# Optimization experiments

Measured on AMD Instinct MI355X. Metric: run time of the kernel, lower is better.

Reference implementation:

```python
import jax, jax.numpy as jnp
import numpy as np

RES = 0.1
TABLE = 1 << 20  # hash_table_size, power of two
PRIMES = np.array([73856093, 19349669, 83492791], dtype=np.int64)
FEAT_DIM = 120
BMIN = (-2.6, -8.1, 0.0)
BMAX = (4.6, 4.7, 3.1)
M_QUERIES = 1_000_000
CORNERS = np.array([[0,0,0],[1,0,0],[0,1,0],[0,0,1],[1,1,0],[1,0,1],[0,1,1],[1,1,1]], dtype=np.int32)


def _build_table():
    # Replicates build_hash_grid(): first-come voxel index per hash slot, collisions skipped.
    xs = np.arange(BMIN[0], BMAX[0], RES, dtype=np.float32)
    ys = np.arange(BMIN[1], BMAX[1], RES, dtype=np.float32)
    zs = np.arange(BMIN[2], BMAX[2], RES, dtype=np.float32)
    gx, gy, gz = np.meshgrid(xs, ys, zs, indexing='ij')
    coords = np.stack([gx, gy, gz], -1).reshape(-1, 3)
    gc = np.floor(coords / RES).astype(np.int64)
    h = np.remainder((gc * PRIMES).sum(-1), TABLE)
    n = coords.shape[0]
    buf = np.full(TABLE, -1, dtype=np.int32)
    buf[h[::-1]] = np.arange(n, dtype=np.int32)[::-1]
    return buf, n


def setup_inputs() -> dict:
    key = jax.random.key(0)
    k1, k2 = jax.random.split(key)
    buf, n_vox = _build_table()
    lo = jnp.array(BMIN, jnp.float32)
    hi = jnp.array(BMAX, jnp.float32)
    query_pts = lo + (hi - lo) * jax.random.uniform(k1, (M_QUERIES, 3), dtype=jnp.float32)
    features = 0.01 * jax.random.normal(k2, (n_vox, FEAT_DIM), dtype=jnp.float32)
    return {
        "query_pts": query_pts,
        "features": features,
        "buffer_voxel_index": jnp.asarray(buf),  # int32 [TABLE]
    }


def reference(query_pts, features, buffer_voxel_index):
    """query_voxel_feature with trilinear_feat=True: 8-corner hash lookup + trilinear blend."""
    primes_u = jnp.asarray(PRIMES.astype(np.uint32))
    gcf = query_pts / RES                        # [M,3]
    floor = jnp.floor(gcf)
    frac = gcf - floor                           # [M,3]
    base = floor.astype(jnp.int32)               # [M,3]
    acc = jnp.zeros((query_pts.shape[0], features.shape[1]), dtype=features.dtype)
    for c in CORNERS:                            # fixed 8-iteration corner loop
        cj = jnp.asarray(c)
        cc = base + cj                           # [M,3]
        # TABLE is a power of two, so low-20-bits of wrapping uint32 arithmetic
        # equals the exact int64 remainder used by torch.
        h = ((cc.astype(jnp.uint32) * primes_u).sum(-1) & (TABLE - 1)).astype(jnp.int32)
        vidx = buffer_voxel_index[h]             # [M], -1 for empty slots
        w = jnp.where(cj == 0, 1.0 - frac, frac).prod(-1)  # [M] trilinear weight
        w = jnp.where(vidx >= 0, w, 0.0)
        acc = acc + features[jnp.maximum(vidx, 0)] * w[:, None]
    return acc
```

## Files before the change

kernel.cpp:

```cpp
#include <hip/hip_runtime.h>


#define TABLE_MASK ((1u << 20) - 1u)
#define FEAT_DIM 120
#define ROW_STRIDE 120
#define NROWS 75
#define NCHUNK 30
#define NXCD 8
#define C8 32

#define NBINS_X 32
#define NBINS_Y 64
#define NBINS_Z 16
#define NBINS (NBINS_X * NBINS_Y * NBINS_Z)

typedef float f4 __attribute__((ext_vector_type(4)));

__device__ __forceinline__ int query_key_from_pt(float px, float py, float pz) {
    const int bx = (int)floorf(px / 0.1f);
    const int by = (int)floorf(py / 0.1f);
    const int bz = (int)floorf(pz / 0.1f);
    const int kx = ((bx + 32) >> 2) & (NBINS_X - 1);
    const int ky = ((by + 96) >> 2) & (NBINS_Y - 1);
    const int kz = (bz >> 1) & (NBINS_Z - 1);
    return ((kx * NBINS_Y) + ky) * NBINS_Z + kz;
}

__global__ __launch_bounds__(256) void zero_kernel(int* __restrict__ hist8) {
    const int i = blockIdx.x * blockDim.x + threadIdx.x;
    if (i < NXCD * NBINS + 1) hist8[i] = 0;
}

__global__ __launch_bounds__(256) void bin_kernel(
    const float* __restrict__ qp, int* __restrict__ hist8,
    f4* __restrict__ sq8, f4* __restrict__ ovf, int Cr, int M)
{
    const int q = blockIdx.x * blockDim.x + threadIdx.x;
    if (q >= M) return;

    int xcd;
    asm volatile("s_getreg_b32 %0, hwreg(HW_REG_XCC_ID)" : "=s"(xcd));
    xcd &= (NXCD - 1);

    const float px = qp[3 * q + 0];
    const float py = qp[3 * q + 1];
    const float pz = qp[3 * q + 2];
    const int key = query_key_from_pt(px, py, pz);

    const int pos = __hip_atomic_fetch_add(&hist8[xcd * NBINS + key], 1,
                                           __ATOMIC_RELAXED,
                                           __HIP_MEMORY_SCOPE_WORKGROUP);
    f4 s;
    s.x = px; s.y = py; s.z = pz; s.w = __int_as_float(q);
    if (pos < Cr) {
        sq8[((size_t)xcd * NBINS + key) * C8 + pos] = s;
    } else {
        const int o = atomicAdd(&hist8[NXCD * NBINS], 1);
        if (o < M) ovf[o] = s;
    }
}

__global__ __launch_bounds__(512) void voxel_trilinear_kernel(
    const f4*    __restrict__ sq8,
    const float* __restrict__ feat,
    const int*   __restrict__ table,
    const int*   __restrict__ hist8,
    float*       __restrict__ out,
    int Cr)
{
    const int x = blockIdx.x & 7, sblk = blockIdx.x >> 3;
    const int wg = (x + ((sblk >> 7) << 3)) * 128 + (sblk & 127);

    __shared__ int   cnt_s[NXCD];
    __shared__ int   pre_s[NXCD + 1];
    __shared__ int   vox[NROWS];
    __shared__ f4    sqL[NXCD * C8];
    __shared__ float rows[NROWS * ROW_STRIDE];

    const int t = threadIdx.x;

    if (t < NXCD) {
        int c = hist8[t * NBINS + wg];
        cnt_s[t] = (c > Cr) ? Cr : c;
    }
    __syncthreads();
    if (t == 0) {
        int acc = 0;
        pre_s[0] = 0;
#pragma unroll
        for (int i = 0; i < NXCD; ++i) { acc += cnt_s[i]; pre_s[i + 1] = acc; }
    }
    __syncthreads();
    const int total = pre_s[NXCD];
    if (total == 0) return;

    const int binx = wg >> 10;
    const int biny = (wg >> 4) & 63;
    const int binz = wg & 15;
    const int vx0 = binx * 4 - 32;
    const int vy0 = biny * 4 - 96;
    const int vz0 = binz * 2;

    if (t < NROWS) {
        const int i = t / 15;
        const int j = (t / 3) % 5;
        const int k = t % 3;
        const unsigned h = (unsigned)(vx0 + i) * 73856093u
                         + (unsigned)(vy0 + j) * 19349669u
                         + (unsigned)(vz0 + k) * 83492791u;
        vox[t] = table[h & TABLE_MASK];
    }
    {
        const int w = t >> 6;
        const int lane = t & 63;
        if (lane < cnt_s[w])
            sqL[pre_s[w] + lane] = sq8[((size_t)w * NBINS + wg) * C8 + lane];
    }
    __syncthreads();

    for (int idx = t; idx < NROWS * NCHUNK; idx += 512) {
        const int row = idx / NCHUNK;
        const int chunk = idx - row * NCHUNK;
        const int v = vox[row];
        f4 val = (f4)(0.0f);
        if (v >= 0)
            val = *reinterpret_cast<const f4*>(feat + (size_t)v * FEAT_DIM + chunk * 4);
        *reinterpret_cast<f4*>(rows + row * ROW_STRIDE + chunk * 4) = val;
    }
    __syncthreads();

    const int group = t >> 4;
    const int l = t & 15;

    for (int qs = group; qs < total; qs += 32) {
        const f4 qv = sqL[qs];
        const float px = qv.x, py = qv.y, pz = qv.z;
        const int q = __float_as_int(qv.w);

        const float gx = px / 0.1f;
        const float gy = py / 0.1f;
        const float gz = pz / 0.1f;
        const float flx = floorf(gx), fly = floorf(gy), flz = floorf(gz);
        const float rx = gx - flx, ry = gy - fly, rz = gz - flz;
        const int bx = (int)flx, by = (int)fly, bz = (int)flz;
        const int lx = (bx + 32) & 3;
        const int ly = (by + 96) & 3;
        const int lz = bz & 1;

        const float sxw = 1.0f - rx, syw = 1.0f - ry, szw = 1.0f - rz;
        float w[8];
        w[0] = sxw * syw * szw;
        w[1] = rx  * syw * szw;
        w[2] = sxw * ry  * szw;
        w[3] = sxw * syw * rz;
        w[4] = rx  * ry  * szw;
        w[5] = rx  * syw * rz;
        w[6] = sxw * ry  * rz;
        w[7] = rx  * ry  * rz;
        const int CX[8] = {0, 1, 0, 0, 1, 1, 0, 1};
        const int CY[8] = {0, 0, 1, 0, 1, 0, 1, 1};
        const int CZ[8] = {0, 0, 0, 1, 0, 1, 1, 1};

        f4 a0 = (f4)(0.0f), a1 = (f4)(0.0f);
#pragma unroll
        for (int k = 0; k < 8; ++k) {
            const int row = ((lx + CX[k]) * 5 + (ly + CY[k])) * 3 + (lz + CZ[k]);
            const float* rp = rows + row * ROW_STRIDE;
            const f4 fa = *reinterpret_cast<const f4*>(rp + l * 4);
            const f4 fb = *reinterpret_cast<const f4*>(rp + 56 + l * 4);
            a0 += fa * w[k];
            a1 += fb * w[k];
        }

        float* po = out + (size_t)q * FEAT_DIM;
        __builtin_nontemporal_store(a0, reinterpret_cast<f4*>(po + l * 4));
        if (l >= 2)
            __builtin_nontemporal_store(a1, reinterpret_cast<f4*>(po + 56 + l * 4));
    }
}

__global__ __launch_bounds__(256) void ovf_kernel(
    const f4*    __restrict__ ovf,
    const int*   __restrict__ hist8,
    const float* __restrict__ feat,
    const int*   __restrict__ table,
    float*       __restrict__ out,
    int M)
{
    int n = hist8[NXCD * NBINS];
    if (n > M) n = M;
    if (n == 0) return;

    const int nthreads = gridDim.x * 256;
    for (int i = blockIdx.x * 256 + threadIdx.x; i < n * 16; i += nthreads) {
        const int g = i >> 4;
        const int l = i & 15;
        const f4 qv = ovf[g];
        const float gx = qv.x / 0.1f;
        const float gy = qv.y / 0.1f;
        const float gz = qv.z / 0.1f;
        const int q = __float_as_int(qv.w);
        const float flx = floorf(gx), fly = floorf(gy), flz = floorf(gz);
        const float rx = gx - flx, ry = gy - fly, rz = gz - flz;
        const int bx = (int)flx, by = (int)fly, bz = (int)flz;

        const unsigned hx0 = (unsigned)bx * 73856093u;
        const unsigned hy0 = (unsigned)by * 19349669u;
        const unsigned hz0 = (unsigned)bz * 83492791u;
        const unsigned hx1 = hx0 + 73856093u;
        const unsigned hy1 = hy0 + 19349669u;
        const unsigned hz1 = hz0 + 83492791u;

        unsigned h[8];
        h[0] = (hx0 + hy0 + hz0) & TABLE_MASK;
        h[1] = (hx1 + hy0 + hz0) & TABLE_MASK;
        h[2] = (hx0 + hy1 + hz0) & TABLE_MASK;
        h[3] = (hx0 + hy0 + hz1) & TABLE_MASK;
        h[4] = (hx1 + hy1 + hz0) & TABLE_MASK;
        h[5] = (hx1 + hy0 + hz1) & TABLE_MASK;
        h[6] = (hx0 + hy1 + hz1) & TABLE_MASK;
        h[7] = (hx1 + hy1 + hz1) & TABLE_MASK;

        int vidx[8];
#pragma unroll
        for (int k = 0; k < 8; ++k) vidx[k] = table[h[k]];

        const float sxw = 1.0f - rx, syw = 1.0f - ry, szw = 1.0f - rz;
        float w[8];
        w[0] = sxw * syw * szw;
        w[1] = rx  * syw * szw;
        w[2] = sxw * ry  * szw;
        w[3] = sxw * syw * rz;
        w[4] = rx  * ry  * szw;
        w[5] = rx  * syw * rz;
        w[6] = sxw * ry  * rz;
        w[7] = rx  * ry  * rz;

        f4 a0 = (f4)(0.0f), a1 = (f4)(0.0f);
#pragma unroll
        for (int k = 0; k < 8; ++k) {
            const int v = vidx[k] >= 0 ? vidx[k] : 0;
            const float wk = vidx[k] >= 0 ? w[k] : 0.0f;
            const float* rp = feat + (size_t)v * FEAT_DIM;
            const f4 fa = *reinterpret_cast<const f4*>(rp + l * 4);
            const f4 fb = *reinterpret_cast<const f4*>(rp + 56 + l * 4);
            a0 += fa * wk;
            a1 += fb * wk;
        }

        float* po = out + (size_t)q * FEAT_DIM;
        __builtin_nontemporal_store(a0, reinterpret_cast<f4*>(po + l * 4));
        if (l >= 2)
            __builtin_nontemporal_store(a1, reinterpret_cast<f4*>(po + 56 + l * 4));
    }
}

extern "C" void kernel_launch(void* const* d_in, const int* in_sizes, int n_in,
                              void* d_out, int out_size, void* d_ws, size_t ws_size,
                              hipStream_t stream) {
    const float* qp    = (const float*)d_in[0];
    const float* feat  = (const float*)d_in[1];
    const int*   table = (const int*)d_in[2];
    float*       out   = (float*)d_out;

    const int M = in_sizes[0] / 3;

    const size_t histB = ((NXCD * NBINS + 1) * sizeof(int) + 15) & ~(size_t)15;
    int* hist8 = (int*)d_ws;
    f4*  ovf   = (f4*)((char*)d_ws + histB);
    f4*  sq8   = ovf + M;

    const size_t fixed = histB + (size_t)M * 16;
    size_t cap = (ws_size > fixed)
               ? (ws_size - fixed) / ((size_t)NXCD * NBINS * 16) : 0;
    int Cr = (cap > C8) ? C8 : (int)cap;
    if (Cr < 1) Cr = 1;

    const int block = 256;
    zero_kernel<<<(NXCD * NBINS + 1 + block - 1) / block, block, 0, stream>>>(hist8);
    bin_kernel<<<(M + block - 1) / block, block, 0, stream>>>(qp, hist8, sq8, ovf, Cr, M);
    voxel_trilinear_kernel<<<NBINS, 512, 0, stream>>>(sq8, feat, table, hist8, out, Cr);
    ovf_kernel<<<512, 256, 0, stream>>>(ovf, hist8, feat, table, out, M);
}
```

Measured before the change: 241.6 us.

## Stage voxel feature rows in LDS as bf16 and halve workgroup size

Feature rows staged in shared memory are converted from fp32 to packed bf16 with a padded row stride, roughly halving LDS footprint and raising occupancy. The workgroup shrinks from 512 to 256 threads, and each lane now handles 8 contiguous features instead of two split f4 chunks. This reduces LDS traffic and bank pressure in the 8-corner gather but loses precision, since features are rounded to bf16 before blending, which may exceed tolerance.

```diff
diff --git a/kernel.cpp b/kernel.cpp
--- a/kernel.cpp
+++ b/kernel.cpp
@@ -3,9 +3,8 @@
 
 #define TABLE_MASK ((1u << 20) - 1u)
 #define FEAT_DIM 120
-#define ROW_STRIDE 120
 #define NROWS 75
-#define NCHUNK 30
+#define RSTRIDE 136
 #define NXCD 8
 #define C8 32
 
@@ -15,6 +14,7 @@
 #define NBINS (NBINS_X * NBINS_Y * NBINS_Z)
 
 typedef float f4 __attribute__((ext_vector_type(4)));
+typedef unsigned u4 __attribute__((ext_vector_type(4)));
 
 __device__ __forceinline__ int query_key_from_pt(float px, float py, float pz) {
     const int bx = (int)floorf(px / 0.1f);
@@ -60,7 +60,7 @@
     }
 }
 
-__global__ __launch_bounds__(512) void voxel_trilinear_kernel(
+__global__ __launch_bounds__(256) void voxel_trilinear_kernel(
     const f4*    __restrict__ sq8,
     const float* __restrict__ feat,
     const int*   __restrict__ table,
@@ -71,11 +71,11 @@
     const int x = blockIdx.x & 7, sblk = blockIdx.x >> 3;
     const int wg = (x + ((sblk >> 7) << 3)) * 128 + (sblk & 127);
 
-    __shared__ int   cnt_s[NXCD];
-    __shared__ int   pre_s[NXCD + 1];
-    __shared__ int   vox[NROWS];
-    __shared__ f4    sqL[NXCD * C8];
-    __shared__ float rows[NROWS * ROW_STRIDE];
+    __shared__ int cnt_s[NXCD];
+    __shared__ int pre_s[NXCD + 1];
+    __shared__ int vox[NROWS];
+    __shared__ f4  sqL[NXCD * C8];
+    __shared__ __align__(16) unsigned short rows[NROWS * RSTRIDE];
 
     const int t = threadIdx.x;
 
@@ -111,28 +111,38 @@
         vox[t] = table[h & TABLE_MASK];
     }
     {
-        const int w = t >> 6;
-        const int lane = t & 63;
-        if (lane < cnt_s[w])
-            sqL[pre_s[w] + lane] = sq8[((size_t)w * NBINS + wg) * C8 + lane];
+        const int seg = t >> 5;
+        const int lane32 = t & 31;
+        if (lane32 < cnt_s[seg])
+            sqL[pre_s[seg] + lane32] = sq8[((size_t)seg * NBINS + wg) * C8 + lane32];
     }
     __syncthreads();
 
-    for (int idx = t; idx < NROWS * NCHUNK; idx += 512) {
-        const int row = idx / NCHUNK;
-        const int chunk = idx - row * NCHUNK;
+    for (int idx = t; idx < NROWS * 15; idx += 256) {
+        const int row = idx / 15;
+        const int c = idx - row * 15;
         const int v = vox[row];
-        f4 val = (f4)(0.0f);
-        if (v >= 0)
-            val = *reinterpret_cast<const f4*>(feat + (size_t)v * FEAT_DIM + chunk * 4);
-        *reinterpret_cast<f4*>(rows + row * ROW_STRIDE + chunk * 4) = val;
+        unsigned u0 = 0, u1 = 0, u2 = 0, u3 = 0;
+        if (v >= 0) {
+            const float* p = feat + (size_t)v * FEAT_DIM + c * 8;
+            const f4 fa = *reinterpret_cast<const f4*>(p);
+            const f4 fb = *reinterpret_cast<const f4*>(p + 4);
+            asm("v_cvt_pk_bf16_f32 %0, %1, %2" : "=v"(u0) : "v"(fa[0]), "v"(fa[1]));
+            asm("v_cvt_pk_bf16_f32 %0, %1, %2" : "=v"(u1) : "v"(fa[2]), "v"(fa[3]));
+            asm("v_cvt_pk_bf16_f32 %0, %1, %2" : "=v"(u2) : "v"(fb[0]), "v"(fb[1]));
+            asm("v_cvt_pk_bf16_f32 %0, %1, %2" : "=v"(u3) : "v"(fb[2]), "v"(fb[3]));
+        }
+        u4 u = {u0, u1, u2, u3};
+        *reinterpret_cast<u4*>(
+            reinterpret_cast<char*>(rows) + row * (RSTRIDE * 2) + c * 16) = u;
     }
     __syncthreads();
 
     const int group = t >> 4;
     const int l = t & 15;
-
-    for (int qs = group; qs < total; qs += 32) {
+    const int le = (l < 15) ? l : 14;
+
+    for (int qs = group; qs < total; qs += 16) {
         const f4 qv = sqL[qs];
         const float px = qv.x, py = qv.y, pz = qv.z;
         const int q = __float_as_int(qv.w);
@@ -165,17 +175,26 @@
 #pragma unroll
         for (int k = 0; k < 8; ++k) {
             const int row = ((lx + CX[k]) * 5 + (ly + CY[k])) * 3 + (lz + CZ[k]);
-            const float* rp = rows + row * ROW_STRIDE;
-            const f4 fa = *reinterpret_cast<const f4*>(rp + l * 4);
-            const f4 fb = *reinterpret_cast<const f4*>(rp + 56 + l * 4);
+            const u4 u = *reinterpret_cast<const u4*>(
+                reinterpret_cast<const char*>(rows) + row * (RSTRIDE * 2) + le * 16);
+            f4 fa, fb;
+            fa[0] = __uint_as_float(u[0] << 16);
+            fa[1] = __uint_as_float(u[0] & 0xffff0000u);
+            fa[2] = __uint_as_float(u[1] << 16);
+            fa[3] = __uint_as_float(u[1] & 0xffff0000u);
+            fb[0] = __uint_as_float(u[2] << 16);
+            fb[1] = __uint_as_float(u[2] & 0xffff0000u);
+            fb[2] = __uint_as_float(u[3] << 16);
+            fb[3] = __uint_as_float(u[3] & 0xffff0000u);
             a0 += fa * w[k];
             a1 += fb * w[k];
         }
 
-        float* po = out + (size_t)q * FEAT_DIM;
-        __builtin_nontemporal_store(a0, reinterpret_cast<f4*>(po + l * 4));
-        if (l >= 2)
-            __builtin_nontemporal_store(a1, reinterpret_cast<f4*>(po + 56 + l * 4));
+        if (l < 15) {
+            float* po = out + (size_t)q * FEAT_DIM + l * 8;
+            __builtin_nontemporal_store(a0, reinterpret_cast<f4*>(po));
+            __builtin_nontemporal_store(a1, reinterpret_cast<f4*>(po + 4));
+        }
     }
 }
 
@@ -279,6 +298,6 @@
     const int block = 256;
     zero_kernel<<<(NXCD * NBINS + 1 + block - 1) / block, block, 0, stream>>>(hist8);
     bin_kernel<<<(M + block - 1) / block, block, 0, stream>>>(qp, hist8, sq8, ovf, Cr, M);
-    voxel_trilinear_kernel<<<NBINS, 512, 0, stream>>>(sq8, feat, table, hist8, out, Cr);
+    voxel_trilinear_kernel<<<NBINS, 256, 0, stream>>>(sq8, feat, table, hist8, out, Cr);
     ovf_kernel<<<512, 256, 0, stream>>>(ovf, hist8, feat, table, out, M);
 }
```

Measured after the change: 271.6 us. +12.4%, slower.

## Sub-bin queries by voxel cell and reuse corner feature rows in registers

Applied to the files above, without the earlier changes.

Queries within each bin are now sub-sorted by their voxel cell using shared-memory atomics and a prefix scan. 16-lane groups grab whole cells through an atomic work counter, load the 8 corner feature chunks into registers once, and loop over every query in that cell, which cuts repeated LDS reads. The bin kernel stores pre-scaled grid coordinates so later stages skip the divide. Launch bounds now request 4 waves per SIMD. Costs include an extra barrier, atomic scheduling overhead and load imbalance when cell counts are uneven.

```diff
diff --git a/kernel.cpp b/kernel.cpp
--- a/kernel.cpp
+++ b/kernel.cpp
@@ -16,16 +16,6 @@
 
 typedef float f4 __attribute__((ext_vector_type(4)));
 
-__device__ __forceinline__ int query_key_from_pt(float px, float py, float pz) {
-    const int bx = (int)floorf(px / 0.1f);
-    const int by = (int)floorf(py / 0.1f);
-    const int bz = (int)floorf(pz / 0.1f);
-    const int kx = ((bx + 32) >> 2) & (NBINS_X - 1);
-    const int ky = ((by + 96) >> 2) & (NBINS_Y - 1);
-    const int kz = (bz >> 1) & (NBINS_Z - 1);
-    return ((kx * NBINS_Y) + ky) * NBINS_Z + kz;
-}
-
 __global__ __launch_bounds__(256) void zero_kernel(int* __restrict__ hist8) {
     const int i = blockIdx.x * blockDim.x + threadIdx.x;
     if (i < NXCD * NBINS + 1) hist8[i] = 0;
@@ -42,16 +32,22 @@
     asm volatile("s_getreg_b32 %0, hwreg(HW_REG_XCC_ID)" : "=s"(xcd));
     xcd &= (NXCD - 1);
 
-    const float px = qp[3 * q + 0];
-    const float py = qp[3 * q + 1];
-    const float pz = qp[3 * q + 2];
-    const int key = query_key_from_pt(px, py, pz);
+    const float gx = qp[3 * q + 0] / 0.1f;
+    const float gy = qp[3 * q + 1] / 0.1f;
+    const float gz = qp[3 * q + 2] / 0.1f;
+    const int bx = (int)floorf(gx);
+    const int by = (int)floorf(gy);
+    const int bz = (int)floorf(gz);
+    const int kx = ((bx + 32) >> 2) & (NBINS_X - 1);
+    const int ky = ((by + 96) >> 2) & (NBINS_Y - 1);
+    const int kz = (bz >> 1) & (NBINS_Z - 1);
+    const int key = ((kx * NBINS_Y) + ky) * NBINS_Z + kz;
 
     const int pos = __hip_atomic_fetch_add(&hist8[xcd * NBINS + key], 1,
                                            __ATOMIC_RELAXED,
                                            __HIP_MEMORY_SCOPE_WORKGROUP);
     f4 s;
-    s.x = px; s.y = py; s.z = pz; s.w = __int_as_float(q);
+    s.x = gx; s.y = gy; s.z = gz; s.w = __int_as_float(q);
     if (pos < Cr) {
         sq8[((size_t)xcd * NBINS + key) * C8 + pos] = s;
     } else {
@@ -60,7 +56,7 @@
     }
 }
 
-__global__ __launch_bounds__(512) void voxel_trilinear_kernel(
+__global__ __launch_bounds__(512, 4) void voxel_trilinear_kernel(
     const f4*    __restrict__ sq8,
     const float* __restrict__ feat,
     const int*   __restrict__ table,
@@ -72,27 +68,27 @@
     const int wg = (x + ((sblk >> 7) << 3)) * 128 + (sblk & 127);
 
     __shared__ int   cnt_s[NXCD];
-    __shared__ int   pre_s[NXCD + 1];
     __shared__ int   vox[NROWS];
-    __shared__ f4    sqL[NXCD * C8];
+    __shared__ int   vcnt[32];
+    __shared__ int   vstart[32];
+    __shared__ int   nextv;
+    __shared__ f4    sqV[NXCD * C8];
     __shared__ float rows[NROWS * ROW_STRIDE];
 
     const int t = threadIdx.x;
 
-    if (t < NXCD) {
-        int c = hist8[t * NBINS + wg];
-        cnt_s[t] = (c > Cr) ? Cr : c;
-    }
+    if (t >= 448 && t < 448 + NXCD) {
+        int c = hist8[(t - 448) * NBINS + wg];
+        cnt_s[t - 448] = (c > Cr) ? Cr : c;
+    }
+    if (t >= 96 && t < 128) vcnt[t - 96] = 0;
+    if (t == 128) nextv = 0;
     __syncthreads();
-    if (t == 0) {
-        int acc = 0;
-        pre_s[0] = 0;
-#pragma unroll
-        for (int i = 0; i < NXCD; ++i) { acc += cnt_s[i]; pre_s[i + 1] = acc; }
-    }
-    __syncthreads();
-    const int total = pre_s[NXCD];
-    if (total == 0) return;
+
+    int tot = 0;
+#pragma unroll
+    for (int i = 0; i < NXCD; ++i) tot += cnt_s[i];
+    if (tot == 0) return;
 
     const int binx = wg >> 10;
     const int biny = (wg >> 4) & 63;
@@ -101,20 +97,28 @@
     const int vy0 = biny * 4 - 96;
     const int vz0 = binz * 2;
 
-    if (t < NROWS) {
-        const int i = t / 15;
-        const int j = (t / 3) % 5;
-        const int k = t % 3;
+    f4 qv_reg;
+    int lid = -1, mypos = 0;
+    if (t >= 256 && t < 256 + NROWS) {
+        const int r = t - 256;
+        const int i = r / 15;
+        const int j = (r / 3) % 5;
+        const int k = r % 3;
         const unsigned h = (unsigned)(vx0 + i) * 73856093u
                          + (unsigned)(vy0 + j) * 19349669u
                          + (unsigned)(vz0 + k) * 83492791u;
-        vox[t] = table[h & TABLE_MASK];
-    }
-    {
-        const int w = t >> 6;
-        const int lane = t & 63;
-        if (lane < cnt_s[w])
-            sqL[pre_s[w] + lane] = sq8[((size_t)w * NBINS + wg) * C8 + lane];
+        vox[r] = table[h & TABLE_MASK];
+    }
+    if (t < 256) {
+        const int seg = t >> 5, lane32 = t & 31;
+        if (lane32 < cnt_s[seg]) {
+            qv_reg = sq8[((size_t)seg * NBINS + wg) * C8 + lane32];
+            const int lx = ((int)floorf(qv_reg.x) + 32) & 3;
+            const int ly = ((int)floorf(qv_reg.y) + 96) & 3;
+            const int lz = (int)floorf(qv_reg.z) & 1;
+            lid = lx * 8 + ly * 2 + lz;
+            mypos = atomicAdd(&vcnt[lid], 1);
+        }
     }
     __syncthreads();
 
@@ -127,55 +131,97 @@
             val = *reinterpret_cast<const f4*>(feat + (size_t)v * FEAT_DIM + chunk * 4);
         *reinterpret_cast<f4*>(rows + row * ROW_STRIDE + chunk * 4) = val;
     }
+    if (t == 0) {
+        int acc = 0;
+#pragma unroll
+        for (int i = 0; i < 32; ++i) { vstart[i] = acc; acc += vcnt[i]; }
+    }
     __syncthreads();
 
-    const int group = t >> 4;
+    if (lid >= 0) sqV[vstart[lid] + mypos] = qv_reg;
+    __syncthreads();
+
     const int l = t & 15;
-
-    for (int qs = group; qs < total; qs += 32) {
-        const f4 qv = sqL[qs];
-        const float px = qv.x, py = qv.y, pz = qv.z;
-        const int q = __float_as_int(qv.w);
-
-        const float gx = px / 0.1f;
-        const float gy = py / 0.1f;
-        const float gz = pz / 0.1f;
-        const float flx = floorf(gx), fly = floorf(gy), flz = floorf(gz);
-        const float rx = gx - flx, ry = gy - fly, rz = gz - flz;
-        const int bx = (int)flx, by = (int)fly, bz = (int)flz;
-        const int lx = (bx + 32) & 3;
-        const int ly = (by + 96) & 3;
-        const int lz = bz & 1;
-
-        const float sxw = 1.0f - rx, syw = 1.0f - ry, szw = 1.0f - rz;
-        float w[8];
-        w[0] = sxw * syw * szw;
-        w[1] = rx  * syw * szw;
-        w[2] = sxw * ry  * szw;
-        w[3] = sxw * syw * rz;
-        w[4] = rx  * ry  * szw;
-        w[5] = rx  * syw * rz;
-        w[6] = sxw * ry  * rz;
-        w[7] = rx  * ry  * rz;
-        const int CX[8] = {0, 1, 0, 0, 1, 1, 0, 1};
-        const int CY[8] = {0, 0, 1, 0, 1, 0, 1, 1};
-        const int CZ[8] = {0, 0, 0, 1, 0, 1, 1, 1};
-
-        f4 a0 = (f4)(0.0f), a1 = (f4)(0.0f);
-#pragma unroll
-        for (int k = 0; k < 8; ++k) {
-            const int row = ((lx + CX[k]) * 5 + (ly + CY[k])) * 3 + (lz + CZ[k]);
-            const float* rp = rows + row * ROW_STRIDE;
-            const f4 fa = *reinterpret_cast<const f4*>(rp + l * 4);
-            const f4 fb = *reinterpret_cast<const f4*>(rp + 56 + l * 4);
-            a0 += fa * w[k];
-            a1 += fb * w[k];
+    const int CX[8] = {0, 1, 0, 0, 1, 1, 0, 1};
+    const int CY[8] = {0, 0, 1, 0, 1, 0, 1, 1};
+    const int CZ[8] = {0, 0, 0, 1, 0, 1, 1, 1};
+
+    for (;;) {
+        int v;
+        if ((t & 15) == 0) v = atomicAdd(&nextv, 1);
+        v = __shfl(v, (t & 63) & ~15);
+        if (v >= 32) break;
+        const int cv = vcnt[v];
+        if (cv == 0) continue;
+        const int vs = vstart[v];
+        const int lx = v >> 3, ly = (v >> 1) & 3, lz = v & 1;
+
+        int ro[8];
+#pragma unroll
+        for (int k = 0; k < 8; ++k)
+            ro[k] = (((lx + CX[k]) * 5 + (ly + CY[k])) * 3 + (lz + CZ[k])) * ROW_STRIDE;
+
+        {
+            f4 fr0, fr1, fr2, fr3, fr4, fr5, fr6, fr7;
+            fr0 = *reinterpret_cast<const f4*>(rows + ro[0] + l * 4);
+            fr1 = *reinterpret_cast<const f4*>(rows + ro[1] + l * 4);
+            fr2 = *reinterpret_cast<const f4*>(rows + ro[2] + l * 4);
+            fr3 = *reinterpret_cast<const f4*>(rows + ro[3] + l * 4);
+            fr4 = *reinterpret_cast<const f4*>(rows + ro[4] + l * 4);
+            fr5 = *reinterpret_cast<const f4*>(rows + ro[5] + l * 4);
+            fr6 = *reinterpret_cast<const f4*>(rows + ro[6] + l * 4);
+            fr7 = *reinterpret_cast<const f4*>(rows + ro[7] + l * 4);
+            for (int i = 0; i < cv; ++i) {
+                const f4 qv = sqV[vs + i];
+                const float rx = qv.x - floorf(qv.x);
+                const float ry = qv.y - floorf(qv.y);
+                const float rz = qv.z - floorf(qv.z);
+                const int q = __float_as_int(qv.w);
+                const float sx = 1.0f - rx, sy = 1.0f - ry, sz = 1.0f - rz;
+                f4 a = (f4)(0.0f);
+                a += fr0 * (sx * sy * sz);
+                a += fr1 * (rx * sy * sz);
+                a += fr2 * (sx * ry * sz);
+                a += fr3 * (sx * sy * rz);
+                a += fr4 * (rx * ry * sz);
+                a += fr5 * (rx * sy * rz);
+                a += fr6 * (sx * ry * rz);
+                a += fr7 * (rx * ry * rz);
+                __builtin_nontemporal_store(
+                    a, reinterpret_cast<f4*>(out + (size_t)q * FEAT_DIM + l * 4));
+            }
         }
-
-        float* po = out + (size_t)q * FEAT_DIM;
-        __builtin_nontemporal_store(a0, reinterpret_cast<f4*>(po + l * 4));
-        if (l >= 2)
-            __builtin_nontemporal_store(a1, reinterpret_cast<f4*>(po + 56 + l * 4));
+        {
+            f4 fr0, fr1, fr2, fr3, fr4, fr5, fr6, fr7;
+            fr0 = *reinterpret_cast<const f4*>(rows + ro[0] + 56 + l * 4);
+            fr1 = *reinterpret_cast<const f4*>(rows + ro[1] + 56 + l * 4);
+            fr2 = *reinterpret_cast<const f4*>(rows + ro[2] + 56 + l * 4);
+            fr3 = *reinterpret_cast<const f4*>(rows + ro[3] + 56 + l * 4);
+            fr4 = *reinterpret_cast<const f4*>(rows + ro[4] + 56 + l * 4);
+            fr5 = *reinterpret_cast<const f4*>(rows + ro[5] + 56 + l * 4);
+            fr6 = *reinterpret_cast<const f4*>(rows + ro[6] + 56 + l * 4);
+            fr7 = *reinterpret_cast<const f4*>(rows + ro[7] + 56 + l * 4);
+            for (int i = 0; i < cv; ++i) {
+                const f4 qv = sqV[vs + i];
+                const float rx = qv.x - floorf(qv.x);
+                const float ry = qv.y - floorf(qv.y);
+                const float rz = qv.z - floorf(qv.z);
+                const int q = __float_as_int(qv.w);
+                const float sx = 1.0f - rx, sy = 1.0f - ry, sz = 1.0f - rz;
+                f4 a = (f4)(0.0f);
+                a += fr0 * (sx * sy * sz);
+                a += fr1 * (rx * sy * sz);
+                a += fr2 * (sx * ry * sz);
+                a += fr3 * (sx * sy * rz);
+                a += fr4 * (rx * ry * sz);
+                a += fr5 * (rx * sy * rz);
+                a += fr6 * (sx * ry * rz);
+                a += fr7 * (rx * ry * rz);
+                if (l >= 2)
+                    __builtin_nontemporal_store(
+                        a, reinterpret_cast<f4*>(out + (size_t)q * FEAT_DIM + 56 + l * 4));
+            }
+        }
     }
 }
 
@@ -196,9 +242,7 @@
         const int g = i >> 4;
         const int l = i & 15;
         const f4 qv = ovf[g];
-        const float gx = qv.x / 0.1f;
-        const float gy = qv.y / 0.1f;
-        const float gz = qv.z / 0.1f;
+        const float gx = qv.x, gy = qv.y, gz = qv.z;
         const int q = __float_as_int(qv.w);
         const float flx = floorf(gx), fly = floorf(gy), flz = floorf(gz);
         const float rx = gx - flx, ry = gy - fly, rz = gz - flz;
```

Result: slower. 253.1 us (+4.7%).

## Shrink bins to 2x2x2 voxels, compact active bins, use persistent blocks

Applied to the files above, without the earlier changes.

Bins are shrunk from 4x4x2 to 2x2x2 voxels, so each block stages 27 feature rows instead of 75. Less shared memory per block allows higher occupancy with 256-thread blocks. A new compaction kernel builds a list of non-empty bins, and a fixed grid of persistent blocks walks that list, so empty bins no longer cost a block launch. Query points are stored pre-scaled by the resolution to save a divide. In exchange, per-bin capacity drops to 12 per XCD, which may send more queries to the slower overflow path, and neighbouring bins now reload more of the same feature rows.

```diff
diff --git a/kernel.cpp b/kernel.cpp
--- a/kernel.cpp
+++ b/kernel.cpp
@@ -4,31 +4,21 @@
 #define TABLE_MASK ((1u << 20) - 1u)
 #define FEAT_DIM 120
 #define ROW_STRIDE 120
-#define NROWS 75
+#define NROWS 27
 #define NCHUNK 30
 #define NXCD 8
-#define C8 32
-
-#define NBINS_X 32
-#define NBINS_Y 64
+#define C8 12
+
+#define NBINS_X 64
+#define NBINS_Y 128
 #define NBINS_Z 16
 #define NBINS (NBINS_X * NBINS_Y * NBINS_Z)
 
 typedef float f4 __attribute__((ext_vector_type(4)));
 
-__device__ __forceinline__ int query_key_from_pt(float px, float py, float pz) {
-    const int bx = (int)floorf(px / 0.1f);
-    const int by = (int)floorf(py / 0.1f);
-    const int bz = (int)floorf(pz / 0.1f);
-    const int kx = ((bx + 32) >> 2) & (NBINS_X - 1);
-    const int ky = ((by + 96) >> 2) & (NBINS_Y - 1);
-    const int kz = (bz >> 1) & (NBINS_Z - 1);
-    return ((kx * NBINS_Y) + ky) * NBINS_Z + kz;
-}
-
 __global__ __launch_bounds__(256) void zero_kernel(int* __restrict__ hist8) {
     const int i = blockIdx.x * blockDim.x + threadIdx.x;
-    if (i < NXCD * NBINS + 1) hist8[i] = 0;
+    if (i < NXCD * NBINS + 2) hist8[i] = 0;
 }
 
 __global__ __launch_bounds__(256) void bin_kernel(
@@ -42,16 +32,22 @@
     asm volatile("s_getreg_b32 %0, hwreg(HW_REG_XCC_ID)" : "=s"(xcd));
     xcd &= (NXCD - 1);
 
-    const float px = qp[3 * q + 0];
-    const float py = qp[3 * q + 1];
-    const float pz = qp[3 * q + 2];
-    const int key = query_key_from_pt(px, py, pz);
+    const float gx = qp[3 * q + 0] / 0.1f;
+    const float gy = qp[3 * q + 1] / 0.1f;
+    const float gz = qp[3 * q + 2] / 0.1f;
+    const int bx = (int)floorf(gx);
+    const int by = (int)floorf(gy);
+    const int bz = (int)floorf(gz);
+    const int kx = ((bx + 32) >> 1) & (NBINS_X - 1);
+    const int ky = ((by + 96) >> 1) & (NBINS_Y - 1);
+    const int kz = (bz >> 1) & (NBINS_Z - 1);
+    const int key = ((kx * NBINS_Y) + ky) * NBINS_Z + kz;
 
     const int pos = __hip_atomic_fetch_add(&hist8[xcd * NBINS + key], 1,
                                            __ATOMIC_RELAXED,
                                            __HIP_MEMORY_SCOPE_WORKGROUP);
     f4 s;
-    s.x = px; s.y = py; s.z = pz; s.w = __int_as_float(q);
+    s.x = gx; s.y = gy; s.z = gz; s.w = __int_as_float(q);
     if (pos < Cr) {
         sq8[((size_t)xcd * NBINS + key) * C8 + pos] = s;
     } else {
@@ -60,17 +56,31 @@
     }
 }
 
-__global__ __launch_bounds__(512) void voxel_trilinear_kernel(
+__global__ __launch_bounds__(256) void compact_kernel(
+    const int* __restrict__ hist8, int* __restrict__ nact,
+    int* __restrict__ list)
+{
+    const int i = blockIdx.x * blockDim.x + threadIdx.x;
+    if (i >= NBINS) return;
+    int tot = 0;
+#pragma unroll
+    for (int s = 0; s < NXCD; ++s) tot += hist8[s * NBINS + i];
+    if (tot > 0) {
+        const int p = atomicAdd(nact, 1);
+        list[p] = i;
+    }
+}
+
+__global__ __launch_bounds__(256, 8) void voxel_trilinear_kernel(
     const f4*    __restrict__ sq8,
     const float* __restrict__ feat,
     const int*   __restrict__ table,
     const int*   __restrict__ hist8,
+    const int*   __restrict__ nactp,
+    const int*   __restrict__ list,
     float*       __restrict__ out,
     int Cr)
 {
-    const int x = blockIdx.x & 7, sblk = blockIdx.x >> 3;
-    const int wg = (x + ((sblk >> 7) << 3)) * 128 + (sblk & 127);
-
     __shared__ int   cnt_s[NXCD];
     __shared__ int   pre_s[NXCD + 1];
     __shared__ int   vox[NROWS];
@@ -78,74 +88,152 @@
     __shared__ float rows[NROWS * ROW_STRIDE];
 
     const int t = threadIdx.x;
-
-    if (t < NXCD) {
-        int c = hist8[t * NBINS + wg];
-        cnt_s[t] = (c > Cr) ? Cr : c;
-    }
-    __syncthreads();
-    if (t == 0) {
-        int acc = 0;
-        pre_s[0] = 0;
-#pragma unroll
-        for (int i = 0; i < NXCD; ++i) { acc += cnt_s[i]; pre_s[i + 1] = acc; }
-    }
-    __syncthreads();
-    const int total = pre_s[NXCD];
-    if (total == 0) return;
-
-    const int binx = wg >> 10;
-    const int biny = (wg >> 4) & 63;
-    const int binz = wg & 15;
-    const int vx0 = binx * 4 - 32;
-    const int vy0 = biny * 4 - 96;
-    const int vz0 = binz * 2;
-
-    if (t < NROWS) {
-        const int i = t / 15;
-        const int j = (t / 3) % 5;
-        const int k = t % 3;
-        const unsigned h = (unsigned)(vx0 + i) * 73856093u
-                         + (unsigned)(vy0 + j) * 19349669u
-                         + (unsigned)(vz0 + k) * 83492791u;
-        vox[t] = table[h & TABLE_MASK];
-    }
-    {
-        const int w = t >> 6;
-        const int lane = t & 63;
-        if (lane < cnt_s[w])
-            sqL[pre_s[w] + lane] = sq8[((size_t)w * NBINS + wg) * C8 + lane];
-    }
-    __syncthreads();
-
-    for (int idx = t; idx < NROWS * NCHUNK; idx += 512) {
-        const int row = idx / NCHUNK;
-        const int chunk = idx - row * NCHUNK;
-        const int v = vox[row];
-        f4 val = (f4)(0.0f);
-        if (v >= 0)
-            val = *reinterpret_cast<const f4*>(feat + (size_t)v * FEAT_DIM + chunk * 4);
-        *reinterpret_cast<f4*>(rows + row * ROW_STRIDE + chunk * 4) = val;
-    }
-    __syncthreads();
-
-    const int group = t >> 4;
-    const int l = t & 15;
-
-    for (int qs = group; qs < total; qs += 32) {
-        const f4 qv = sqL[qs];
-        const float px = qv.x, py = qv.y, pz = qv.z;
+    const int nact = *nactp;
+
+    for (int bi = blockIdx.x; bi < nact; bi += gridDim.x) {
+        const int wg = list[bi];
+        __syncthreads();
+
+        if (t < NXCD) {
+            int c = hist8[t * NBINS + wg];
+            cnt_s[t] = (c > Cr) ? Cr : c;
+        }
+        __syncthreads();
+        if (t == 0) {
+            int acc = 0;
+            pre_s[0] = 0;
+#pragma unroll
+            for (int i = 0; i < NXCD; ++i) { acc += cnt_s[i]; pre_s[i + 1] = acc; }
+        }
+        __syncthreads();
+        const int total = pre_s[NXCD];
+
+        const int binx = wg >> 11;
+        const int biny = (wg >> 4) & 127;
+        const int binz = wg & 15;
+        const int vx0 = binx * 2 - 32;
+        const int vy0 = biny * 2 - 96;
+        const int vz0 = binz * 2;
+
+        if (t < NROWS) {
+            const int i = t / 9;
+            const int j = (t / 3) % 3;
+            const int k = t % 3;
+            const unsigned h = (unsigned)(vx0 + i) * 73856093u
+                             + (unsigned)(vy0 + j) * 19349669u
+                             + (unsigned)(vz0 + k) * 83492791u;
+            vox[t] = table[h & TABLE_MASK];
+        }
+        if (t >= 128) {
+            const int seg = (t - 128) >> 4;
+            const int lane16 = t & 15;
+            if (lane16 < cnt_s[seg])
+                sqL[pre_s[seg] + lane16] =
+                    sq8[((size_t)seg * NBINS + wg) * C8 + lane16];
+        }
+        __syncthreads();
+
+        for (int idx = t; idx < NROWS * NCHUNK; idx += 256) {
+            const int row = idx / NCHUNK;
+            const int chunk = idx - row * NCHUNK;
+            const int v = vox[row];
+            f4 val = (f4)(0.0f);
+            if (v >= 0)
+                val = *reinterpret_cast<const f4*>(
+                    feat + (size_t)v * FEAT_DIM + chunk * 4);
+            *reinterpret_cast<f4*>(rows + row * ROW_STRIDE + chunk * 4) = val;
+        }
+        __syncthreads();
+
+        const int group = t >> 4;
+        const int l = t & 15;
+        const int CX[8] = {0, 1, 0, 0, 1, 1, 0, 1};
+        const int CY[8] = {0, 0, 1, 0, 1, 0, 1, 1};
+        const int CZ[8] = {0, 0, 0, 1, 0, 1, 1, 1};
+
+        for (int qs = group; qs < total; qs += 16) {
+            const f4 qv = sqL[qs];
+            const float rx = qv.x - floorf(qv.x);
+            const float ry = qv.y - floorf(qv.y);
+            const float rz = qv.z - floorf(qv.z);
+            const int q = __float_as_int(qv.w);
+            const int lx = ((int)floorf(qv.x) + 32) & 1;
+            const int ly = ((int)floorf(qv.y) + 96) & 1;
+            const int lz = (int)floorf(qv.z) & 1;
+
+            const float sx = 1.0f - rx, sy = 1.0f - ry, sz = 1.0f - rz;
+            float w[8];
+            w[0] = sx * sy * sz;
+            w[1] = rx * sy * sz;
+            w[2] = sx * ry * sz;
+            w[3] = sx * sy * rz;
+            w[4] = rx * ry * sz;
+            w[5] = rx * sy * rz;
+            w[6] = sx * ry * rz;
+            w[7] = rx * ry * rz;
+
+            f4 a0 = (f4)(0.0f), a1 = (f4)(0.0f);
+#pragma unroll
+            for (int k = 0; k < 8; ++k) {
+                const int row = ((lx + CX[k]) * 3 + (ly + CY[k])) * 3 + (lz + CZ[k]);
+                const float* rp = rows + row * ROW_STRIDE;
+                const f4 fa = *reinterpret_cast<const f4*>(rp + l * 4);
+                const f4 fb = *reinterpret_cast<const f4*>(rp + 56 + l * 4);
+                a0 += fa * w[k];
+                a1 += fb * w[k];
+            }
+
+            float* po = out + (size_t)q * FEAT_DIM;
+            __builtin_nontemporal_store(a0, reinterpret_cast<f4*>(po + l * 4));
+            if (l >= 2)
+                __builtin_nontemporal_store(a1, reinterpret_cast<f4*>(po + 56 + l * 4));
+        }
+    }
+}
+
+__global__ __launch_bounds__(256) void ovf_kernel(
+    const f4*    __restrict__ ovf,
+    const int*   __restrict__ hist8,
+    const float* __restrict__ feat,
+    const int*   __restrict__ table,
+    float*       __restrict__ out,
+    int M)
+{
+    int n = hist8[NXCD * NBINS];
+    if (n > M) n = M;
+    if (n == 0) return;
+
+    const int nthreads = gridDim.x * 256;
+    for (int i = blockIdx.x * 256 + threadIdx.x; i < n * 16; i += nthreads) {
+        const int g = i >> 4;
+        const int l = i & 15;
+        const f4 qv = ovf[g];
+        const float gx = qv.x, gy = qv.y, gz = qv.z;
         const int q = __float_as_int(qv.w);
-
-        const float gx = px / 0.1f;
-        const float gy = py / 0.1f;
-        const float gz = pz / 0.1f;
         const float flx = floorf(gx), fly = floorf(gy), flz = floorf(gz);
         const float rx = gx - flx, ry = gy - fly, rz = gz - flz;
         const int bx = (int)flx, by = (int)fly, bz = (int)flz;
-        const int lx = (bx + 32) & 3;
-        const int ly = (by + 96) & 3;
-        const int lz = bz & 1;
+
+        const unsigned hx0 = (unsigned)bx * 73856093u;
+        const unsigned hy0 = (unsigned)by * 19349669u;
+        const unsigned hz0 = (unsigned)bz * 83492791u;
+        const unsigned hx1 = hx0 + 73856093u;
+        const unsigned hy1 = hy0 + 19349669u;
+        const unsigned hz1 = hz0 + 83492791u;
+
+        unsigned h[8];
+        h[0] = (hx0 + hy0 + hz0) & TABLE_MASK;
+        h[1] = (hx1 + hy0 + hz0) & TABLE_MASK;
+        h[2] = (hx0 + hy1 + hz0) & TABLE_MASK;
+        h[3] = (hx0 + hy0 + hz1) & TABLE_MASK;
+        h[4] = (hx1 + hy1 + hz0) & TABLE_MASK;
+        h[5] = (hx1 + hy0 + hz1) & TABLE_MASK;
+        h[6] = (hx0 + hy1 + hz1) & TABLE_MASK;
+        h[7] = (hx1 + hy1 + hz1) & TABLE_MASK;
+
+        int vidx[8];
+#pragma unroll
+        for (int k = 0; k < 8; ++k) vidx[k] = table[h[k]];
 
         const float sxw = 1.0f - rx, syw = 1.0f - ry, szw = 1.0f - rz;
         float w[8];
@@ -157,84 +245,6 @@
         w[5] = rx  * syw * rz;
         w[6] = sxw * ry  * rz;
         w[7] = rx  * ry  * rz;
-        const int CX[8] = {0, 1, 0, 0, 1, 1, 0, 1};
-        const int CY[8] = {0, 0, 1, 0, 1, 0, 1, 1};
-        const int CZ[8] = {0, 0, 0, 1, 0, 1, 1, 1};
-
-        f4 a0 = (f4)(0.0f), a1 = (f4)(0.0f);
-#pragma unroll
-        for (int k = 0; k < 8; ++k) {
-            const int row = ((lx + CX[k]) * 5 + (ly + CY[k])) * 3 + (lz + CZ[k]);
-            const float* rp = rows + row * ROW_STRIDE;
-            const f4 fa = *reinterpret_cast<const f4*>(rp + l * 4);
-            const f4 fb = *reinterpret_cast<const f4*>(rp + 56 + l * 4);
-            a0 += fa * w[k];
-            a1 += fb * w[k];
-        }
-
-        float* po = out + (size_t)q * FEAT_DIM;
-        __builtin_nontemporal_store(a0, reinterpret_cast<f4*>(po + l * 4));
-        if (l >= 2)
-            __builtin_nontemporal_store(a1, reinterpret_cast<f4*>(po + 56 + l * 4));
-    }
-}
-
-__global__ __launch_bounds__(256) void ovf_kernel(
-    const f4*    __restrict__ ovf,
-    const int*   __restrict__ hist8,
-    const float* __restrict__ feat,
-    const int*   __restrict__ table,
-    float*       __restrict__ out,
-    int M)
-{
-    int n = hist8[NXCD * NBINS];
-    if (n > M) n = M;
-    if (n == 0) return;
-
-    const int nthreads = gridDim.x * 256;
-    for (int i = blockIdx.x * 256 + threadIdx.x; i < n * 16; i += nthreads) {
-        const int g = i >> 4;
-        const int l = i & 15;
-        const f4 qv = ovf[g];
-        const float gx = qv.x / 0.1f;
-        const float gy = qv.y / 0.1f;
-        const float gz = qv.z / 0.1f;
-        const int q = __float_as_int(qv.w);
-        const float flx = floorf(gx), fly = floorf(gy), flz = floorf(gz);
-        const float rx = gx - flx, ry = gy - fly, rz = gz - flz;
-        const int bx = (int)flx, by = (int)fly, bz = (int)flz;
-
-        const unsigned hx0 = (unsigned)bx * 73856093u;
-        const unsigned hy0 = (unsigned)by * 19349669u;
-        const unsigned hz0 = (unsigned)bz * 83492791u;
-        const unsigned hx1 = hx0 + 73856093u;
-        const unsigned hy1 = hy0 + 19349669u;
-        const unsigned hz1 = hz0 + 83492791u;
-
-        unsigned h[8];
-        h[0] = (hx0 + hy0 + hz0) & TABLE_MASK;
-        h[1] = (hx1 + hy0 + hz0) & TABLE_MASK;
-        h[2] = (hx0 + hy1 + hz0) & TABLE_MASK;
-        h[3] = (hx0 + hy0 + hz1) & TABLE_MASK;
-        h[4] = (hx1 + hy1 + hz0) & TABLE_MASK;
-        h[5] = (hx1 + hy0 + hz1) & TABLE_MASK;
-        h[6] = (hx0 + hy1 + hz1) & TABLE_MASK;
-        h[7] = (hx1 + hy1 + hz1) & TABLE_MASK;
-
-        int vidx[8];
-#pragma unroll
-        for (int k = 0; k < 8; ++k) vidx[k] = table[h[k]];
-
-        const float sxw = 1.0f - rx, syw = 1.0f - ry, szw = 1.0f - rz;
-        float w[8];
-        w[0] = sxw * syw * szw;
-        w[1] = rx  * syw * szw;
-        w[2] = sxw * ry  * szw;
-        w[3] = sxw * syw * rz;
-        w[4] = rx  * ry  * szw;
-        w[5] = rx  * syw * rz;
-        w[6] = sxw * ry  * rz;
-        w[7] = rx  * ry  * rz;
 
         f4 a0 = (f4)(0.0f), a1 = (f4)(0.0f);
 #pragma unroll
@@ -265,20 +275,25 @@
 
     const int M = in_sizes[0] / 3;
 
-    const size_t histB = ((NXCD * NBINS + 1) * sizeof(int) + 15) & ~(size_t)15;
+    const size_t histB = ((NXCD * NBINS + 2) * sizeof(int) + 15) & ~(size_t)15;
+    const size_t listB = (NBINS * sizeof(int) + 15) & ~(size_t)15;
     int* hist8 = (int*)d_ws;
-    f4*  ovf   = (f4*)((char*)d_ws + histB);
+    int* nact  = hist8 + NXCD * NBINS + 1;
+    int* list  = (int*)((char*)d_ws + histB);
+    f4*  ovf   = (f4*)((char*)d_ws + histB + listB);
     f4*  sq8   = ovf + M;
 
-    const size_t fixed = histB + (size_t)M * 16;
+    const size_t fixed = histB + listB + (size_t)M * 16;
     size_t cap = (ws_size > fixed)
                ? (ws_size - fixed) / ((size_t)NXCD * NBINS * 16) : 0;
     int Cr = (cap > C8) ? C8 : (int)cap;
     if (Cr < 1) Cr = 1;
 
     const int block = 256;
-    zero_kernel<<<(NXCD * NBINS + 1 + block - 1) / block, block, 0, stream>>>(hist8);
+    zero_kernel<<<(NXCD * NBINS + 2 + block - 1) / block, block, 0, stream>>>(hist8);
     bin_kernel<<<(M + block - 1) / block, block, 0, stream>>>(qp, hist8, sq8, ovf, Cr, M);
-    voxel_trilinear_kernel<<<NBINS, 512, 0, stream>>>(sq8, feat, table, hist8, out, Cr);
+    compact_kernel<<<(NBINS + block - 1) / block, block, 0, stream>>>(hist8, nact, list);
+    voxel_trilinear_kernel<<<2048, 256, 0, stream>>>(sq8, feat, table, hist8,
+                                                     nact, list, out, Cr);
     ovf_kernel<<<512, 256, 0, stream>>>(ovf, hist8, feat, table, out, M);
 }
```

Measured after the change: 261.4 us. 1.08x slower.
